# Kernel optimization log

Measured on AMD Instinct MI355X. Metric: run time of the kernel, lower is better.

The kernel has to match this reference:

```python
import jax, jax.numpy as jnp
import numpy as np

B, S, E, NH = 4, 4096, 2048, 16
HD = E // NH


def setup_inputs() -> dict:
    key = jax.random.key(0)
    ks = jax.random.split(key, 10)
    sc = 0.02  # keep linear outputs well-scaled
    return {
        "x": jax.random.normal(ks[0], (B, S, E), dtype=jnp.float32),
        "alpha": jax.random.uniform(ks[1], (1,), dtype=jnp.float32),
        "Wq": jax.random.normal(ks[2], (E, E), dtype=jnp.float32) * sc,
        "bq": jax.random.normal(ks[3], (E,), dtype=jnp.float32) * sc,
        "Wk": jax.random.normal(ks[4], (E, E), dtype=jnp.float32) * sc,
        "bk": jax.random.normal(ks[5], (E,), dtype=jnp.float32) * sc,
        "Wv": jax.random.normal(ks[6], (E, E), dtype=jnp.float32) * sc,
        "bv": jax.random.normal(ks[7], (E,), dtype=jnp.float32) * sc,
        "Wfc": jax.random.normal(ks[8], (E, E), dtype=jnp.float32) * sc,
        "bfc": jax.random.normal(ks[9], (E,), dtype=jnp.float32) * sc,
    }


def _split_heads(t):
    # [b, s, (nh hd)] -> [b, nh, s, hd]
    b, s, _ = t.shape
    return t.reshape(b, s, NH, HD).transpose(0, 2, 1, 3)


def reference(x, alpha, Wq, bq, Wk, bk, Wv, bv, Wfc, bfc):
    q = _split_heads(x @ Wq + bq)  # [b, nh, s, hd]
    k = _split_heads(x @ Wk + bk)
    v = _split_heads(x @ Wv + bv)
    # K^T K  : [b, nh, hd, hd]
    kk = jnp.einsum('bhsd,bhse->bhde', k, k)
    kk = kk + alpha[0] * jnp.eye(HD, dtype=kk.dtype)
    kk_inv = jnp.linalg.inv(kk)
    # (alpha I + K^T K)^-1 K^T V : [b, nh, hd, hd]
    ktv = jnp.einsum('bhsd,bhse->bhde', k, v)
    score = jax.nn.softmax(kk_inv @ ktv, axis=-1)
    out = jnp.einsum('bhsd,bhde->bhse', q, score)  # [b, nh, s, hd]
    out = out.transpose(0, 2, 1, 3).reshape(x.shape[0], x.shape[1], E)
    return out @ Wfc + bfc
```

## Files before the change

### kernel.cpp

```cpp
#include <hip/hip_runtime.h>
#include <hip/hip_bf16.h>


typedef __attribute__((ext_vector_type(4))) float  f32x4;
typedef __attribute__((ext_vector_type(8))) short  s16x8;

__device__ __forceinline__ unsigned short f2bf(float f) {
  unsigned u = __float_as_uint(f);
  unsigned r = (u + 0x7FFFu + ((u >> 16) & 1u)) >> 16;
  return (unsigned short)r;
}
__device__ __forceinline__ float bf2f(unsigned short u) {
  return __uint_as_float(((unsigned)u) << 16);
}

__device__ __forceinline__ void gld16(const void* g, void* l) {
  __builtin_amdgcn_global_load_lds(
      (const __attribute__((address_space(1))) unsigned int*)g,
      (__attribute__((address_space(3))) unsigned int*)l,
      16, 0, 0);
}

__global__ void cast_x_kernel(const float* __restrict__ x,
                              unsigned short* __restrict__ xb, long n) {
  long i = ((long)blockIdx.x * blockDim.x + threadIdx.x) * 4;
  if (i < n) {
    float4 v = *(const float4*)(x + i);
    ushort4 o;
    o.x = f2bf(v.x); o.y = f2bf(v.y); o.z = f2bf(v.z); o.w = f2bf(v.w);
    *(ushort4*)(xb + i) = o;
  }
}

__global__ void transw_kernel(const float* __restrict__ Wq, const float* __restrict__ Wk,
                              const float* __restrict__ Wv, const float* __restrict__ Wfc,
                              unsigned short* __restrict__ wqkv_t,
                              unsigned short* __restrict__ wfc_t) {
  __shared__ float tile[32][33];
  int z = blockIdx.z;
  const float* W = (z == 0) ? Wq : (z == 1) ? Wk : (z == 2) ? Wv : Wfc;
  unsigned short* dst = (z < 3) ? (wqkv_t + (size_t)z * 2048 * 2048) : wfc_t;
  int x0 = blockIdx.x * 32, y0 = blockIdx.y * 32;
  int tx = threadIdx.x & 31, ty = threadIdx.x >> 5;
#pragma unroll
  for (int r = 0; r < 4; ++r)
    tile[ty + r * 8][tx] = W[(size_t)(y0 + ty + r * 8) * 2048 + x0 + tx];
  __syncthreads();
#pragma unroll
  for (int r = 0; r < 4; ++r)
    dst[(size_t)(x0 + ty + r * 8) * 2048 + y0 + tx] = f2bf(tile[tx][ty + r * 8]);
}

__global__ void bias_kernel(const float* __restrict__ bq, const float* __restrict__ bk,
                            const float* __restrict__ bv, float* __restrict__ bqkv) {
  int i = blockIdx.x * 256 + threadIdx.x;
  bqkv[i] = (i < 2048) ? bq[i] : (i < 4096) ? bk[i - 2048] : bv[i - 4096];
}

__global__ __launch_bounds__(256, 2)
void qkv_gemm(const unsigned short* __restrict__ A,
              const unsigned short* __restrict__ Bw,
              const float* __restrict__ bias,
              unsigned short* __restrict__ qbuf,
              unsigned short* __restrict__ Kt,
              unsigned short* __restrict__ Vt) {
  __shared__ __align__(16) unsigned short As[128 * 64];
  __shared__ __align__(16) unsigned short Bs[128 * 64];
  const int t = threadIdx.x;
  const int lane = t & 63;
  const int w = t >> 6;
  const int wr = (w >> 1) * 64, wc = (w & 1) * 64;
  const int l15 = lane & 15, lq = lane >> 4;
  const int sxor = l15 & 7;
  const unsigned short* Ab = A + (size_t)blockIdx.y * 128 * 2048;
  const unsigned short* Bb = Bw + (size_t)blockIdx.x * 128 * 2048;

  f32x4 acc[4][4] = {};
  const int srow = t >> 3;
  const int scol = (((t & 7) ^ (srow & 7))) * 8;

  for (int kt = 0; kt < 32; ++kt) {
    const unsigned short* Ag = Ab + kt * 64 + (size_t)srow * 2048 + scol;
    const unsigned short* Bg = Bb + kt * 64 + (size_t)srow * 2048 + scol;
    __syncthreads();
#pragma unroll
    for (int i = 0; i < 4; ++i) {
      gld16(Ag + (size_t)(32 * i) * 2048, As + t * 8 + i * 2048);
      gld16(Bg + (size_t)(32 * i) * 2048, Bs + t * 8 + i * 2048);
    }
    __syncthreads();
#pragma unroll
    for (int ks = 0; ks < 2; ++ks) {
      const int ca = ((ks * 4 + lq) ^ sxor) * 8;
      s16x8 af[4], bf[4];
#pragma unroll
      for (int i = 0; i < 4; ++i) {
        af[i] = *(const s16x8*)(As + (wr + i * 16 + l15) * 64 + ca);
        bf[i] = *(const s16x8*)(Bs + (wc + i * 16 + l15) * 64 + ca);
      }
#pragma unroll
      for (int i = 0; i < 4; ++i)
#pragma unroll
        for (int j = 0; j < 4; ++j)
          acc[i][j] = __builtin_amdgcn_mfma_f32_16x16x32_bf16(af[i], bf[j], acc[i][j], 0, 0, 0);
    }
  }
  const int row0 = blockIdx.y * 128 + wr + lq * 4;
  const int col0 = blockIdx.x * 128 + wc + l15;
  const int region = blockIdx.x >> 4;
  if (region == 0) {
#pragma unroll
    for (int j = 0; j < 4; ++j) {
      int col = col0 + j * 16;
      float bv = bias[col];
#pragma unroll
      for (int i = 0; i < 4; ++i)
#pragma unroll
        for (int r = 0; r < 4; ++r)
          qbuf[(size_t)(row0 + i * 16 + r) * 2048 + col] = f2bf(acc[i][j][r] + bv);
    }
  } else {
    unsigned short* T = (region == 1) ? Kt : Vt;
#pragma unroll
    for (int j = 0; j < 4; ++j) {
      int col = col0 + j * 16;
      float bv = bias[col];
      int d = col & 127;
      int h = (col >> 7) & 15;
#pragma unroll
      for (int i = 0; i < 4; ++i) {
        int row = row0 + i * 16;
        int b = row >> 12, s = row & 4095;
        ushort4 u;
        u.x = f2bf(acc[i][j][0] + bv);
        u.y = f2bf(acc[i][j][1] + bv);
        u.z = f2bf(acc[i][j][2] + bv);
        u.w = f2bf(acc[i][j][3] + bv);
        *(ushort4*)(T + (size_t)(b * 16 + h) * 524288 + (size_t)d * 4096 + s) = u;
      }
    }
  }
}

__global__ __launch_bounds__(256, 2)
void kk_gemm(const unsigned short* __restrict__ Kt,
             const unsigned short* __restrict__ Vt,
             float* __restrict__ kk, float* __restrict__ ktv) {
  __shared__ __align__(16) unsigned short As[128 * 64];
  __shared__ __align__(16) unsigned short Bs[128 * 64];
  const int t = threadIdx.x;
  const int lane = t & 63;
  const int w = t >> 6;
  const int wr = (w >> 1) * 64, wc = (w & 1) * 64;
  const int l15 = lane & 15, lq = lane >> 4;
  const int sxor = l15 & 7;
  const int bh = blockIdx.z & 63;
  const int op = (blockIdx.z >> 6) & 1;
  const int split = blockIdx.z >> 7;
  const unsigned short* Ab = Kt + (size_t)bh * 524288 + split * 1024;
  const unsigned short* Bb = (op ? Vt : Kt) + (size_t)bh * 524288 + split * 1024;
  float* C = (op ? ktv : kk) + (size_t)bh * 16384;

  f32x4 acc[4][4] = {};
  const int srow = t >> 3;
  const int scol = (((t & 7) ^ (srow & 7))) * 8;

  for (int kt = 0; kt < 16; ++kt) {
    const unsigned short* Ag = Ab + kt * 64 + (size_t)srow * 4096 + scol;
    const unsigned short* Bg = Bb + kt * 64 + (size_t)srow * 4096 + scol;
    __syncthreads();
#pragma unroll
    for (int i = 0; i < 4; ++i) {
      gld16(Ag + (size_t)(32 * i) * 4096, As + t * 8 + i * 2048);
      gld16(Bg + (size_t)(32 * i) * 4096, Bs + t * 8 + i * 2048);
    }
    __syncthreads();
#pragma unroll
    for (int ks = 0; ks < 2; ++ks) {
      const int ca = ((ks * 4 + lq) ^ sxor) * 8;
      s16x8 af[4], bf[4];
#pragma unroll
      for (int i = 0; i < 4; ++i) {
        af[i] = *(const s16x8*)(As + (wr + i * 16 + l15) * 64 + ca);
        bf[i] = *(const s16x8*)(Bs + (wc + i * 16 + l15) * 64 + ca);
      }
#pragma unroll
      for (int i = 0; i < 4; ++i)
#pragma unroll
        for (int j = 0; j < 4; ++j)
          acc[i][j] = __builtin_amdgcn_mfma_f32_16x16x32_bf16(af[i], bf[j], acc[i][j], 0, 0, 0);
    }
  }
  const int row0 = wr + lq * 4;
  const int col0 = wc + l15;
#pragma unroll
  for (int j = 0; j < 4; ++j)
#pragma unroll
    for (int i = 0; i < 4; ++i)
#pragma unroll
      for (int r = 0; r < 4; ++r)
        atomicAdd(&C[(row0 + i * 16 + r) * 128 + col0 + j * 16], acc[i][j][r]);
}

template <bool OUT_BF16, bool HAS_BIAS>
__global__ __launch_bounds__(256, 2)
void gemm_bt(const unsigned short* __restrict__ A, int lda,
             const unsigned short* __restrict__ B, int ldb,
             const float* __restrict__ bias,
             void* __restrict__ C, int ldc, int K,
             long sAb, long sAh, long sBb, long sBh, long sCb, long sCh,
             int nhmod) {
  __shared__ __align__(16) unsigned short As[128 * 64];
  __shared__ __align__(16) unsigned short Bs[128 * 64];
  const int t = threadIdx.x;
  const int lane = t & 63;
  const int w = t >> 6;
  const int wr = (w >> 1) * 64, wc = (w & 1) * 64;
  const int l15 = lane & 15, lq = lane >> 4;
  const int sxor = l15 & 7;
  const int zb = blockIdx.z / nhmod, zh = blockIdx.z - zb * nhmod;
  const unsigned short* Ab = A + zb * sAb + zh * sAh + (size_t)blockIdx.y * 128 * lda;
  const unsigned short* Bb = B + zb * sBb + zh * sBh + (size_t)blockIdx.x * 128 * ldb;

  f32x4 acc[4][4] = {};
  const int nk = K >> 6;
  const int srow = t >> 3;
  const int scol = (((t & 7) ^ (srow & 7))) * 8;

  for (int kt = 0; kt < nk; ++kt) {
    const unsigned short* Ag = Ab + kt * 64 + (size_t)srow * lda + scol;
    const unsigned short* Bg = Bb + kt * 64 + (size_t)srow * ldb + scol;
    __syncthreads();
#pragma unroll
    for (int i = 0; i < 4; ++i) {
      gld16(Ag + (size_t)(32 * i) * lda, As + t * 8 + i * 2048);
      gld16(Bg + (size_t)(32 * i) * ldb, Bs + t * 8 + i * 2048);
    }
    __syncthreads();
#pragma unroll
    for (int ks = 0; ks < 2; ++ks) {
      const int ca = ((ks * 4 + lq) ^ sxor) * 8;
      s16x8 af[4], bf[4];
#pragma unroll
      for (int i = 0; i < 4; ++i) {
        af[i] = *(const s16x8*)(As + (wr + i * 16 + l15) * 64 + ca);
        bf[i] = *(const s16x8*)(Bs + (wc + i * 16 + l15) * 64 + ca);
      }
#pragma unroll
      for (int i = 0; i < 4; ++i)
#pragma unroll
        for (int j = 0; j < 4; ++j)
          acc[i][j] = __builtin_amdgcn_mfma_f32_16x16x32_bf16(af[i], bf[j], acc[i][j], 0, 0, 0);
    }
  }
  const long Cbase = zb * sCb + zh * sCh;
  const long row0 = (long)blockIdx.y * 128 + wr + lq * 4;
  const long col0 = (long)blockIdx.x * 128 + wc + l15;
#pragma unroll
  for (int j = 0; j < 4; ++j) {
    long col = col0 + j * 16;
    float bv = HAS_BIAS ? bias[col] : 0.0f;
#pragma unroll
    for (int i = 0; i < 4; ++i)
#pragma unroll
      for (int r = 0; r < 4; ++r) {
        float v = acc[i][j][r] + bv;
        long idx = Cbase + (row0 + i * 16 + r) * (long)ldc + col;
        if (OUT_BF16) ((unsigned short*)C)[idx] = f2bf(v);
        else          ((float*)C)[idx] = v;
      }
  }
}

__global__ __launch_bounds__(256, 1)
void inv_softmax_kernel(const float* __restrict__ kk, const float* __restrict__ ktv,
                        const float* __restrict__ alphap,
                        unsigned short* __restrict__ score_t) {
  __shared__ __align__(16) float A[128 * 132];
  __shared__ __align__(16) float rowbuf[2][132];
  __shared__ __align__(16) float colbuf[2][132];
  const int bh = blockIdx.x, t = threadIdx.x;
  const float* kkb = kk + (size_t)bh * 16384;
  const float* tvb = ktv + (size_t)bh * 16384;
  const float al = alphap[0];

  for (int i = t; i < 16384; i += 256) {
    int r = i >> 7, c = i & 127;
    A[r * 132 + c] = kkb[i] + ((r == c) ? al : 0.0f);
  }
  __syncthreads();
  if (t < 128) { rowbuf[0][t] = A[t]; colbuf[0][t] = A[t * 132]; }
  __syncthreads();

  const int i2 = t >> 1, half = t & 1;
  const int jb = half * 64;
  for (int k = 0; k < 128; ++k) {
    const float* rb = rowbuf[k & 1];
    float piv = rb[k];
    float d = 1.0f / piv;
    float c = colbuf[k & 1][i2];
    bool isPivRow = (i2 == k);
    float cd = isPivRow ? 0.0f : c * d;
    float scale = isPivRow ? d : 1.0f;
    float* Arow = A + i2 * 132 + jb;
    const float* rbh = rb + jb;
#pragma unroll
    for (int jj = 0; jj < 16; ++jj) {
      float4 r4 = *(const float4*)(rbh + jj * 4);
      float4 v = *(float4*)(Arow + jj * 4);
      v.x = v.x * scale - cd * r4.x;
      v.y = v.y * scale - cd * r4.y;
      v.z = v.z * scale - cd * r4.z;
      v.w = v.w * scale - cd * r4.w;
      *(float4*)(Arow + jj * 4) = v;
    }
    if ((k >> 6) == half) {
      if (!isPivRow) A[i2 * 132 + k] = -c * d;
      else           A[k * 132 + k] = d;
    }
    __syncthreads();
    if (t < 128 && k < 127) {
      rowbuf[(k + 1) & 1][t] = A[(k + 1) * 132 + t];
      colbuf[(k + 1) & 1][t] = A[t * 132 + (k + 1)];
    }
    __syncthreads();
  }

  const int ty2 = t >> 4, tx2 = t & 15;
  float X[8][8] = {};
  for (int f = 0; f < 128; ++f) {
    float av[8];
#pragma unroll
    for (int i = 0; i < 8; ++i) av[i] = A[(ty2 * 8 + i) * 132 + f];
    float4 b0 = *(const float4*)(tvb + f * 128 + tx2 * 8);
    float4 b1 = *(const float4*)(tvb + f * 128 + tx2 * 8 + 4);
#pragma unroll
    for (int i = 0; i < 8; ++i) {
      X[i][0] = fmaf(av[i], b0.x, X[i][0]); X[i][1] = fmaf(av[i], b0.y, X[i][1]);
      X[i][2] = fmaf(av[i], b0.z, X[i][2]); X[i][3] = fmaf(av[i], b0.w, X[i][3]);
      X[i][4] = fmaf(av[i], b1.x, X[i][4]); X[i][5] = fmaf(av[i], b1.y, X[i][5]);
      X[i][6] = fmaf(av[i], b1.z, X[i][6]); X[i][7] = fmaf(av[i], b1.w, X[i][7]);
    }
  }
  __syncthreads();
#pragma unroll
  for (int i = 0; i < 8; ++i) {
    *(float4*)(A + (ty2 * 8 + i) * 132 + tx2 * 8)     = make_float4(X[i][0], X[i][1], X[i][2], X[i][3]);
    *(float4*)(A + (ty2 * 8 + i) * 132 + tx2 * 8 + 4) = make_float4(X[i][4], X[i][5], X[i][6], X[i][7]);
  }
  __syncthreads();
  {
    const int r = t >> 1;
    const float* row = A + r * 132 + (t & 1) * 64;
    float mx = -1e30f;
    for (int j = 0; j < 64; ++j) mx = fmaxf(mx, row[j]);
    mx = fmaxf(mx, __shfl_xor(mx, 1));
    float sum = 0.0f;
    for (int j = 0; j < 64; ++j) sum += __expf(row[j] - mx);
    sum += __shfl_xor(sum, 1);
    float inv = 1.0f / sum;
    unsigned short* outb = score_t + (size_t)bh * 16384 + r;
    const int e0 = (t & 1) * 64;
    for (int j = 0; j < 64; ++j)
      outb[(size_t)(e0 + j) * 128] = f2bf(__expf(row[j] - mx) * inv);
  }
}

extern "C" void kernel_launch(void* const* d_in, const int* in_sizes, int n_in,
                              void* d_out, int out_size, void* d_ws, size_t ws_size,
                              hipStream_t stream) {
  const float* x     = (const float*)d_in[0];
  const float* alpha = (const float*)d_in[1];
  const float* Wq    = (const float*)d_in[2];
  const float* bq    = (const float*)d_in[3];
  const float* Wk    = (const float*)d_in[4];
  const float* bk    = (const float*)d_in[5];
  const float* Wv    = (const float*)d_in[6];
  const float* bv    = (const float*)d_in[7];
  const float* Wfc   = (const float*)d_in[8];
  const float* bfc   = (const float*)d_in[9];
  float* out = (float*)d_out;
  char* ws = (char*)d_ws;

  unsigned short* qbuf   = (unsigned short*)(ws);
  unsigned short* Kt     = (unsigned short*)(ws + 67108864);
  unsigned short* Vt     = (unsigned short*)(ws + 134217728);
  unsigned short* xb     = (unsigned short*)(ws + 201326592);
  float* kkbuf           = (float*)(ws + 201326592);
  float* ktvbuf          = (float*)(ws + 201326592 + 4194304);
  unsigned short* score_t= (unsigned short*)(ws + 201326592 + 8388608);
  unsigned short* outat  = Kt;
  unsigned short* wqkv_t = (unsigned short*)(ws + 268435456);
  unsigned short* wfc_t  = (unsigned short*)(ws + 293601280);
  float* bqkv            = (float*)(ws + 301989888);

  transw_kernel<<<dim3(64, 64, 4), 256, 0, stream>>>(Wq, Wk, Wv, Wfc, wqkv_t, wfc_t);
  cast_x_kernel<<<32768, 256, 0, stream>>>(x, xb, 33554432L);
  bias_kernel<<<24, 256, 0, stream>>>(bq, bk, bv, bqkv);

  qkv_gemm<<<dim3(48, 128, 1), 256, 0, stream>>>(xb, wqkv_t, bqkv, qbuf, Kt, Vt);

  hipMemsetAsync(kkbuf, 0, 8388608, stream);
  kk_gemm<<<dim3(1, 1, 512), 256, 0, stream>>>(Kt, Vt, kkbuf, ktvbuf);

  inv_softmax_kernel<<<64, 256, 0, stream>>>(kkbuf, ktvbuf, alpha, score_t);

  gemm_bt<true, false><<<dim3(1, 32, 64), 256, 0, stream>>>(
      qbuf, 2048, score_t, 128, nullptr, outat, 2048, 128,
      8388608L, 128L,
      262144L, 16384L,
      8388608L, 128L,
      16);

  gemm_bt<false, true><<<dim3(16, 128, 1), 256, 0, stream>>>(
      outat, 2048, wfc_t, 2048, bfc, out, 2048, 2048,
      0, 0, 0, 0, 0, 0, 1);
}
```

Measured before the change: 1.033 ms.

## Replace QKV and output GEMMs with pipelined 256x256-tile double-buffered kernel

New measurement: 1.012 ms. 2.0% less time.

```diff
diff --git a/kernel.cpp b/kernel.cpp
--- a/kernel.cpp
+++ b/kernel.cpp
@@ -57,89 +57,172 @@
   bqkv[i] = (i < 2048) ? bq[i] : (i < 4096) ? bk[i - 2048] : bv[i - 4096];
 }
 
-__global__ __launch_bounds__(256, 2)
-void qkv_gemm(const unsigned short* __restrict__ A,
-              const unsigned short* __restrict__ Bw,
-              const float* __restrict__ bias,
-              unsigned short* __restrict__ qbuf,
-              unsigned short* __restrict__ Kt,
-              unsigned short* __restrict__ Vt) {
-  __shared__ __align__(16) unsigned short As[128 * 64];
-  __shared__ __align__(16) unsigned short Bs[128 * 64];
+#define BARRIER()  asm volatile("s_barrier" ::: "memory")
+#define LGKM0()    asm volatile("s_waitcnt lgkmcnt(0)" ::: "memory")
+#define VMCNT6()   asm volatile("s_waitcnt vmcnt(6)" ::: "memory")
+#define VMCNT0()   asm volatile("s_waitcnt vmcnt(0)" ::: "memory")
+
+template <int MODE>
+__global__ __launch_bounds__(512, 2)
+void gemm256(const unsigned short* __restrict__ A, int lda,
+             const unsigned short* __restrict__ Bw, int ldb,
+             const float* __restrict__ bias,
+             unsigned short* __restrict__ qbuf,
+             unsigned short* __restrict__ Kt,
+             unsigned short* __restrict__ Vt,
+             float* __restrict__ outf, int K) {
+  __shared__ __align__(16) unsigned short sb[65536];
   const int t = threadIdx.x;
   const int lane = t & 63;
   const int w = t >> 6;
-  const int wr = (w >> 1) * 64, wc = (w & 1) * 64;
+  const int wm = w >> 2, wn = w & 3;
   const int l15 = lane & 15, lq = lane >> 4;
-  const int sxor = l15 & 7;
-  const unsigned short* Ab = A + (size_t)blockIdx.y * 128 * 2048;
-  const unsigned short* Bb = Bw + (size_t)blockIdx.x * 128 * 2048;
-
-  f32x4 acc[4][4] = {};
-  const int srow = t >> 3;
-  const int scol = (((t & 7) ^ (srow & 7))) * 8;
-
-  for (int kt = 0; kt < 32; ++kt) {
-    const unsigned short* Ag = Ab + kt * 64 + (size_t)srow * 2048 + scol;
-    const unsigned short* Bg = Bb + kt * 64 + (size_t)srow * 2048 + scol;
-    __syncthreads();
-#pragma unroll
-    for (int i = 0; i < 4; ++i) {
-      gld16(Ag + (size_t)(32 * i) * 2048, As + t * 8 + i * 2048);
-      gld16(Bg + (size_t)(32 * i) * 2048, Bs + t * 8 + i * 2048);
-    }
-    __syncthreads();
-#pragma unroll
-    for (int ks = 0; ks < 2; ++ks) {
-      const int ca = ((ks * 4 + lq) ^ sxor) * 8;
-      s16x8 af[4], bf[4];
-#pragma unroll
-      for (int i = 0; i < 4; ++i) {
-        af[i] = *(const s16x8*)(As + (wr + i * 16 + l15) * 64 + ca);
-        bf[i] = *(const s16x8*)(Bs + (wc + i * 16 + l15) * 64 + ca);
+  const int sx = l15 & 7;
+
+  const unsigned short* Ab = A + (size_t)blockIdx.y * 256 * lda;
+  const unsigned short* Bb = Bw + (size_t)blockIdx.x * 256 * ldb;
+
+  const int sr = t >> 3;
+  const int sc = ((t & 7) ^ (sr & 7)) * 8;
+
+#define STAGE_A(kt, half, buf) do {                                             \
+    const unsigned short* _g = Ab + (size_t)((half) * 128 + sr) * lda + (kt) * 64 + sc; \
+    unsigned short* _l = sb + (buf) * 16384 + (half) * 8192 + t * 8;            \
+    gld16(_g, _l);                                                              \
+    gld16(_g + (size_t)64 * lda, _l + 4096);                                    \
+  } while (0)
+#define STAGE_B(kt, half, buf) do {                                             \
+    const unsigned short* _g = Bb + (size_t)((half) * 128 + sr) * ldb + (kt) * 64 + sc; \
+    unsigned short* _l = sb + 32768 + (buf) * 16384 + (half) * 8192 + t * 8;    \
+    gld16(_g, _l);                                                              \
+    gld16(_g + (size_t)64 * ldb, _l + 4096);                                    \
+  } while (0)
+
+#define LDA_FRAG(mq) do {                                                       \
+    const unsigned short* _a = As_p + (wm * 128 + (mq) * 64 + l15) * 64;        \
+    _Pragma("unroll") for (int i = 0; i < 4; ++i)                               \
+      _Pragma("unroll") for (int ks = 0; ks < 2; ++ks)                          \
+        af[i * 2 + ks] = *(const s16x8*)(_a + i * 1024 + ((ks * 4 + lq) ^ sx) * 8); \
+  } while (0)
+#define LDB_FRAG(dst, nq) do {                                                  \
+    const unsigned short* _b = Bs_p + (wn * 64 + (nq) * 32 + l15) * 64;         \
+    _Pragma("unroll") for (int jj = 0; jj < 2; ++jj)                            \
+      _Pragma("unroll") for (int ks = 0; ks < 2; ++ks)                          \
+        dst[jj * 2 + ks] = *(const s16x8*)(_b + jj * 1024 + ((ks * 4 + lq) ^ sx) * 8); \
+  } while (0)
+#define MMA_Q(mq, nq, bfr) do {                                                 \
+    _Pragma("unroll") for (int i = 0; i < 4; ++i)                               \
+      _Pragma("unroll") for (int jj = 0; jj < 2; ++jj) {                        \
+        acc[(mq) * 4 + i][(nq) * 2 + jj] = __builtin_amdgcn_mfma_f32_16x16x32_bf16( \
+            af[i * 2 + 0], bfr[jj * 2 + 0], acc[(mq) * 4 + i][(nq) * 2 + jj], 0, 0, 0); \
+        acc[(mq) * 4 + i][(nq) * 2 + jj] = __builtin_amdgcn_mfma_f32_16x16x32_bf16( \
+            af[i * 2 + 1], bfr[jj * 2 + 1], acc[(mq) * 4 + i][(nq) * 2 + jj], 0, 0, 0); \
+      }                                                                         \
+  } while (0)
+
+#define KTILE(tile, STG) do {                                                   \
+    const int _p = (tile) & 1;                                                  \
+    const unsigned short* As_p = sb + _p * 16384;                               \
+    const unsigned short* Bs_p = sb + 32768 + _p * 16384;                       \
+    s16x8 af[8], bf0[4], bf1[4];                                                \
+                                                       \
+    LDA_FRAG(0);                                                                \
+    LDB_FRAG(bf0, 0);                                                           \
+    if ((STG) >= 1) STAGE_B((tile) + 1, 1, _p ^ 1);                             \
+    BARRIER(); LGKM0();                                                         \
+    __builtin_amdgcn_s_setprio(1); MMA_Q(0, 0, bf0); __builtin_amdgcn_s_setprio(0); \
+    BARRIER();                                                                  \
+                                                       \
+    LDB_FRAG(bf1, 1);                                                           \
+    BARRIER(); LGKM0();                                                         \
+    __builtin_amdgcn_s_setprio(1); MMA_Q(0, 1, bf1); __builtin_amdgcn_s_setprio(0); \
+    BARRIER();                                                                  \
+                                                       \
+    LDA_FRAG(1);                                                                \
+    if ((STG) == 2) STAGE_B((tile) + 2, 0, _p);                                 \
+    BARRIER(); LGKM0();                                                         \
+    __builtin_amdgcn_s_setprio(1); MMA_Q(1, 1, bf1); __builtin_amdgcn_s_setprio(0); \
+    BARRIER();                                                                  \
+                                                       \
+    if ((STG) == 2) { STAGE_A((tile) + 2, 0, _p); STAGE_A((tile) + 2, 1, _p); VMCNT6(); } \
+    else if ((STG) == 1) { VMCNT0(); }                                          \
+    BARRIER();                                                                  \
+    __builtin_amdgcn_s_setprio(1); MMA_Q(1, 0, bf0); __builtin_amdgcn_s_setprio(0); \
+    BARRIER();                                                                  \
+  } while (0)
+
+  f32x4 acc[8][4] = {};
+  const int nkt = K >> 6;
+
+  STAGE_A(0, 0, 0); STAGE_A(0, 1, 0);
+  STAGE_B(0, 0, 0); STAGE_B(0, 1, 0);
+  STAGE_A(1, 0, 1); STAGE_A(1, 1, 1);
+  STAGE_B(1, 0, 1);
+  VMCNT6();
+  BARRIER();
+
+  for (int tile = 0; tile < nkt - 2; ++tile) { KTILE(tile, 2); }
+  KTILE(nkt - 2, 1);
+  KTILE(nkt - 1, 0);
+
+  const int colb = blockIdx.x * 256 + wn * 64 + l15;
+  const long rowb = (long)blockIdx.y * 256 + wm * 128 + lq * 4;
+  if (MODE == 0) {
+    const int region = blockIdx.x >> 3;
+    if (region == 0) {
+#pragma unroll
+      for (int n = 0; n < 4; ++n) {
+        int col = colb + n * 16;
+        float bv = bias[col];
+#pragma unroll
+        for (int m = 0; m < 8; ++m) {
+          long row = rowb + m * 16;
+#pragma unroll
+          for (int r = 0; r < 4; ++r)
+            qbuf[(row + r) * 2048 + col] = f2bf(acc[m][n][r] + bv);
+        }
       }
-#pragma unroll
-      for (int i = 0; i < 4; ++i)
-#pragma unroll
-        for (int j = 0; j < 4; ++j)
-          acc[i][j] = __builtin_amdgcn_mfma_f32_16x16x32_bf16(af[i], bf[j], acc[i][j], 0, 0, 0);
-    }
-  }
-  const int row0 = blockIdx.y * 128 + wr + lq * 4;
-  const int col0 = blockIdx.x * 128 + wc + l15;
-  const int region = blockIdx.x >> 4;
-  if (region == 0) {
-#pragma unroll
-    for (int j = 0; j < 4; ++j) {
-      int col = col0 + j * 16;
+    } else {
+      unsigned short* T = (region == 1) ? Kt : Vt;
+#pragma unroll
+      for (int n = 0; n < 4; ++n) {
+        int col = colb + n * 16;
+        float bv = bias[col];
+        int cin = col & 2047;
+        int d = cin & 127, h = cin >> 7;
+#pragma unroll
+        for (int m = 0; m < 8; ++m) {
+          long row = rowb + m * 16;
+          int b = (int)(row >> 12), s = (int)(row & 4095);
+          ushort4 u;
+          u.x = f2bf(acc[m][n][0] + bv);
+          u.y = f2bf(acc[m][n][1] + bv);
+          u.z = f2bf(acc[m][n][2] + bv);
+          u.w = f2bf(acc[m][n][3] + bv);
+          *(ushort4*)(T + (size_t)(b * 16 + h) * 524288 + (size_t)d * 4096 + s) = u;
+        }
+      }
+    }
+  } else {
+#pragma unroll
+    for (int n = 0; n < 4; ++n) {
+      int col = colb + n * 16;
       float bv = bias[col];
 #pragma unroll
-      for (int i = 0; i < 4; ++i)
+      for (int m = 0; m < 8; ++m) {
+        long row = rowb + m * 16;
 #pragma unroll
         for (int r = 0; r < 4; ++r)
-          qbuf[(size_t)(row0 + i * 16 + r) * 2048 + col] = f2bf(acc[i][j][r] + bv);
-    }
-  } else {
-    unsigned short* T = (region == 1) ? Kt : Vt;
-#pragma unroll
-    for (int j = 0; j < 4; ++j) {
-      int col = col0 + j * 16;
-      float bv = bias[col];
-      int d = col & 127;
-      int h = (col >> 7) & 15;
-#pragma unroll
-      for (int i = 0; i < 4; ++i) {
-        int row = row0 + i * 16;
-        int b = row >> 12, s = row & 4095;
-        ushort4 u;
-        u.x = f2bf(acc[i][j][0] + bv);
-        u.y = f2bf(acc[i][j][1] + bv);
-        u.z = f2bf(acc[i][j][2] + bv);
-        u.w = f2bf(acc[i][j][3] + bv);
-        *(ushort4*)(T + (size_t)(b * 16 + h) * 524288 + (size_t)d * 4096 + s) = u;
+          outf[(row + r) * 2048 + col] = acc[m][n][r] + bv;
       }
     }
   }
+#undef KTILE
+#undef MMA_Q
+#undef LDB_FRAG
+#undef LDA_FRAG
+#undef STAGE_B
+#undef STAGE_A
 }
 
 __global__ __launch_bounds__(256, 2)
@@ -398,7 +481,8 @@
   cast_x_kernel<<<32768, 256, 0, stream>>>(x, xb, 33554432L);
   bias_kernel<<<24, 256, 0, stream>>>(bq, bk, bv, bqkv);
 
-  qkv_gemm<<<dim3(48, 128, 1), 256, 0, stream>>>(xb, wqkv_t, bqkv, qbuf, Kt, Vt);
+  gemm256<0><<<dim3(24, 64), 512, 0, stream>>>(
+      xb, 2048, wqkv_t, 2048, bqkv, qbuf, Kt, Vt, nullptr, 2048);
 
   hipMemsetAsync(kkbuf, 0, 8388608, stream);
   kk_gemm<<<dim3(1, 1, 512), 256, 0, stream>>>(Kt, Vt, kkbuf, ktvbuf);
@@ -412,7 +496,6 @@
       8388608L, 128L,
       16);
 
-  gemm_bt<false, true><<<dim3(16, 128, 1), 256, 0, stream>>>(
-      outat, 2048, wfc_t, 2048, bfc, out, 2048, 2048,
-      0, 0, 0, 0, 0, 0, 1);
-}
+  gemm256<1><<<dim3(8, 64), 512, 0, stream>>>(
+      outat, 2048, wfc_t, 2048, bfc, nullptr, nullptr, nullptr, out, 2048);
+}
```
